# Optimization experiments

Hardware: AMD Instinct MI355X
Metric: run time of the kernel (lower is better)

The kernel has to match this reference:

```python
import jax, jax.numpy as jnp
import numpy as np

ALPHA, BETA, GAMMA, DELTA = 0.3, 0.3, 0.2, 0.2
BK, BW = 3, 3.0
EPS = 1e-7


def _bce_with_logits(x, y):
    # numerically stable: max(x,0) - x*y + log(1+exp(-|x|)); pos_weight=1.0
    return jnp.maximum(x, 0.0) - x * y + jnp.log1p(jnp.exp(-jnp.abs(x)))


def _lovasz_hinge_flat(x, y):
    # x, y: (N,) flattened logits / binary labels for one image
    signs = 2.0 * y - 1.0
    errors = 1.0 - x * signs
    perm = jnp.argsort(-errors)            # descending sort permutation
    errors_sorted = errors[perm]
    gt_sorted = y[perm]
    gts = gt_sorted.sum()
    intersection = gts - jnp.cumsum(gt_sorted)
    union = gts + jnp.cumsum(1.0 - gt_sorted)
    jaccard = 1.0 - intersection / union
    jaccard = jnp.concatenate([jaccard[:1], jaccard[1:] - jaccard[:-1]])
    return jnp.dot(jax.nn.relu(errors_sorted), jaccard)


def setup_inputs() -> dict:
    key = jax.random.key(0)
    k1, k2 = jax.random.split(key)
    logits = jax.random.normal(k1, (32, 1, 512, 512), dtype=jnp.float32)
    # binary ground-truth mask (0/1 floats)
    targets = jnp.round(jax.random.uniform(k2, (32, 1, 512, 512), dtype=jnp.float32))
    return {"logits": logits, "targets": targets}


def reference(logits, targets):
    # --- BCE term (pos_weight = 1.0) ---
    bce_elem = _bce_with_logits(logits, targets)
    bce = bce_elem.mean()

    # --- Dice term ---
    probs = jax.nn.sigmoid(logits)
    num = 2.0 * (probs * targets).sum(axis=(2, 3))
    den = (probs + targets).sum(axis=(2, 3)) + EPS
    dice = 1.0 - (num / den).mean()

    # --- Boundary-weighted BCE term (weights computed under no_grad) ---
    kernel = jnp.ones((1, 1, BK, BK), logits.dtype) / (BK * BK)
    smooth = jax.lax.conv_general_dilated(
        targets, kernel, window_strides=(1, 1), padding='SAME',
        dimension_numbers=('NCHW', 'OIHW', 'NCHW'))
    edges = ((smooth > 0.01) & (smooth < 0.99)).astype(logits.dtype)
    weights = jax.lax.stop_gradient(1.0 + edges * (BW - 1.0))
    boundary = (bce_elem * weights).mean()

    # --- Lovasz hinge, per image then averaged ---
    B = logits.shape[0]
    lov = jax.vmap(_lovasz_hinge_flat)(
        logits.reshape(B, -1), targets.reshape(B, -1)).mean()

    return ALPHA * bce + BETA * dice + GAMMA * boundary + DELTA * lov
```

## Files before the change

### kernel.cpp

```cpp
#include <hip/hip_runtime.h>
#include <hip/hip_bf16.h>


#define NB      32
#define HH      512
#define WW      512
#define HW      (HH*WW)
#define NTOT    (NB*HW)
#define K_BINS  1024
#define INV_H   128.0f
#define BIN_W   (1.0f/128.0f)

struct Ws {
    unsigned cnt[NB*K_BINS];
    float    sy[NB];
    float    spy[NB];
    float    Pim[NB];
    float    bce_sum;
    float    bceE_sum;
    float    lov_sum;
};

__device__ __forceinline__ void process_elem(float x, float y, float wsum,
                                             float& bce_s, float& bceE_s, float& sy_s,
                                             float& spy_s, float& P_s,
                                             unsigned* s_cnt) {
    const float ax = fabsf(x);
    const float t  = __expf(-ax);
    const float bce = fmaxf(x, 0.f) - x * y + __logf(1.f + t);
    const float inv = __builtin_amdgcn_rcpf(1.f + t);
    const float s = (x >= 0.f) ? inv : t * inv;
    const bool edge = (wsum > 0.5f) && (wsum < 8.5f);

    bce_s  += bce;
    bceE_s += edge ? bce : 0.f;
    sy_s   += s * y;
    spy_s  += s + y;
    P_s    += y;

    const float e = 1.f - x * (2.f * y - 1.f);
    if (e > 0.f) {
        int b = (int)(e * INV_H);
        if (b > K_BINS - 1) b = K_BINS - 1;
        atomicAdd(&s_cnt[b], (y > 0.5f) ? 0x10001u : 1u);
    }
}

__global__ __launch_bounds__(256, 2) void kernelA(const float* __restrict__ logits,
                                                  const float* __restrict__ targets,
                                                  Ws* __restrict__ ws) {
    __shared__ unsigned s_cnt[K_BINS];
    __shared__ float    red[4][5];

    const int tid  = threadIdx.x;
    const int lane = tid & 63;
    const int wave = tid >> 6;
    for (int i = tid; i < K_BINS; i += 256) s_cnt[i] = 0u;
    __syncthreads();

    const int img   = blockIdx.x >> 4;
    const int strip = ((blockIdx.x & 15) << 2) | wave;
    const int r0    = strip * 8;

    const float4* __restrict__ tg4 = (const float4*)(targets + img * HW);
    const float4* __restrict__ lg4 = (const float4*)(logits  + img * HW);
    const int cA = lane;
    const int cB = 64 + lane;

    float4 T[5][2]; float fT[5];
    float4 X[3][2];

#pragma unroll
    for (int s = 0; s < 5; ++s) {
        const int rr = r0 - 1 + s;
        const int rc = rr < 0 ? 0 : (rr > 511 ? 511 : rr);
        fT[s] = (rr >= 0 && rr < 512) ? 1.f : 0.f;
        T[s][0] = tg4[rc * 128 + cA];
        T[s][1] = tg4[rc * 128 + cB];
    }
#pragma unroll
    for (int s = 0; s < 3; ++s) {
        const int rr = r0 + s;
        X[s][0] = lg4[rr * 128 + cA];
        X[s][1] = lg4[rr * 128 + cB];
    }

    float bce_s = 0.f, bceE_s = 0.f, sy_s = 0.f, spy_s = 0.f, P_s = 0.f;

#pragma unroll
    for (int j = 0; j < 8; ++j) {
        const int ia = j % 5, ib = (j + 1) % 5, ic = (j + 2) % 5;
        const int xs = j % 3;
        const float fa = fT[ia], fc = fT[ic];

        float4 csA, csB;
        csA.x = fmaf(T[ia][0].x, fa, fmaf(T[ic][0].x, fc, T[ib][0].x));
        csA.y = fmaf(T[ia][0].y, fa, fmaf(T[ic][0].y, fc, T[ib][0].y));
        csA.z = fmaf(T[ia][0].z, fa, fmaf(T[ic][0].z, fc, T[ib][0].z));
        csA.w = fmaf(T[ia][0].w, fa, fmaf(T[ic][0].w, fc, T[ib][0].w));
        csB.x = fmaf(T[ia][1].x, fa, fmaf(T[ic][1].x, fc, T[ib][1].x));
        csB.y = fmaf(T[ia][1].y, fa, fmaf(T[ic][1].y, fc, T[ib][1].y));
        csB.z = fmaf(T[ia][1].z, fa, fmaf(T[ic][1].z, fc, T[ib][1].z));
        csB.w = fmaf(T[ia][1].w, fa, fmaf(T[ic][1].w, fc, T[ib][1].w));

        const float upA  = __shfl_up(csA.w, 1);
        const float dnA  = __shfl_down(csA.x, 1);
        const float upB  = __shfl_up(csB.w, 1);
        const float dnB  = __shfl_down(csB.x, 1);
        const float bc0  = __shfl(csB.x, 0);
        const float bc63 = __shfl(csA.w, 63);
        const float LA = (lane == 0)  ? 0.f  : upA;
        const float RA = (lane == 63) ? bc0  : dnA;
        const float LB = (lane == 0)  ? bc63 : upB;
        const float RB = (lane == 63) ? 0.f  : dnB;

        process_elem(X[xs][0].x, T[ib][0].x, LA + csA.x + csA.y,    bce_s, bceE_s, sy_s, spy_s, P_s, s_cnt);
        process_elem(X[xs][0].y, T[ib][0].y, csA.x + csA.y + csA.z, bce_s, bceE_s, sy_s, spy_s, P_s, s_cnt);
        process_elem(X[xs][0].z, T[ib][0].z, csA.y + csA.z + csA.w, bce_s, bceE_s, sy_s, spy_s, P_s, s_cnt);
        process_elem(X[xs][0].w, T[ib][0].w, csA.z + csA.w + RA,    bce_s, bceE_s, sy_s, spy_s, P_s, s_cnt);
        process_elem(X[xs][1].x, T[ib][1].x, LB + csB.x + csB.y,    bce_s, bceE_s, sy_s, spy_s, P_s, s_cnt);
        process_elem(X[xs][1].y, T[ib][1].y, csB.x + csB.y + csB.z, bce_s, bceE_s, sy_s, spy_s, P_s, s_cnt);
        process_elem(X[xs][1].z, T[ib][1].z, csB.y + csB.z + csB.w, bce_s, bceE_s, sy_s, spy_s, P_s, s_cnt);
        process_elem(X[xs][1].w, T[ib][1].w, csB.z + csB.w + RB,    bce_s, bceE_s, sy_s, spy_s, P_s, s_cnt);

        if (j < 5) {
            const int rr = r0 + j + 4;
            const int rc = rr > 511 ? 511 : rr;
            fT[ia] = (rr < 512) ? 1.f : 0.f;
            T[ia][0] = tg4[rc * 128 + cA];
            T[ia][1] = tg4[rc * 128 + cB];
            const int rx = r0 + j + 3;
            X[xs][0] = lg4[rx * 128 + cA];
            X[xs][1] = lg4[rx * 128 + cB];
        }
    }
    __syncthreads();

    unsigned* g_c = ws->cnt + img * K_BINS;
    for (int i = tid; i < K_BINS; i += 256) {
        const unsigned cpk = s_cnt[i];
        if (cpk) atomicAdd(&g_c[i], cpk);
    }

    for (int off = 32; off; off >>= 1) {
        bce_s  += __shfl_down(bce_s, off);
        bceE_s += __shfl_down(bceE_s, off);
        sy_s   += __shfl_down(sy_s, off);
        spy_s  += __shfl_down(spy_s, off);
        P_s    += __shfl_down(P_s, off);
    }
    if (lane == 0) {
        red[wave][0] = bce_s; red[wave][1] = bceE_s; red[wave][2] = sy_s;
        red[wave][3] = spy_s; red[wave][4] = P_s;
    }
    __syncthreads();
    if (tid == 0) {
        float a = 0.f, b = 0.f, c2 = 0.f, d = 0.f, e2 = 0.f;
        for (int w = 0; w < 4; ++w) {
            a += red[w][0]; b += red[w][1]; c2 += red[w][2];
            d += red[w][3]; e2 += red[w][4];
        }
        atomicAdd(&ws->bce_sum, a);
        atomicAdd(&ws->bceE_sum, b);
        atomicAdd(&ws->sy[img], c2);
        atomicAdd(&ws->spy[img], d);
        atomicAdd(&ws->Pim[img], e2);
    }
}

__global__ __launch_bounds__(256) void kernelB(Ws* __restrict__ ws) {
    __shared__ unsigned sc_a[256];
    __shared__ unsigned sc_p[256];
    __shared__ double   dred[4];

    const int img = blockIdx.x;
    const int tid = threadIdx.x;
    const unsigned* __restrict__ cn = ws->cnt + img * K_BINS;

    unsigned la[4], lp[4];
    float    me[4];
    unsigned tot_a = 0, tot_p = 0;
#pragma unroll
    for (int j = 0; j < 4; ++j) {
        const int k = K_BINS - 1 - (tid * 4 + j);
        const unsigned cpk = cn[k];
        la[j] = cpk & 0xFFFFu; lp[j] = cpk >> 16;
        me[j] = ((float)k + 0.5f) * BIN_W;
        tot_a += la[j]; tot_p += lp[j];
    }

    sc_a[tid] = tot_a; sc_p[tid] = tot_p;
    __syncthreads();
    for (int off = 1; off < 256; off <<= 1) {
        unsigned va = (tid >= off) ? sc_a[tid - off] : 0u;
        unsigned vp = (tid >= off) ? sc_p[tid - off] : 0u;
        __syncthreads();
        sc_a[tid] += va; sc_p[tid] += vp;
        __syncthreads();
    }
    const unsigned excl_a = sc_a[tid] - tot_a;
    const unsigned excl_p = sc_p[tid] - tot_p;

    const double P = (double)ws->Pim[img];
    double run_a = (double)excl_a, run_p = (double)excl_p;
    double contrib = 0.0;
#pragma unroll
    for (int j = 0; j < 4; ++j) {
        const double m = (double)la[j];
        const double p = (double)lp[j];
        if (la[j]) {
            const double u = P + (run_a + 0.5 * m) - (run_p + 0.5 * p);
            const double c = run_p + 0.5 * p;
            contrib += (double)(lp[j] * me[j]) / u;
            const double den = u * (u - 1.0);
            if (den > 0.0)
                contrib += (double)((la[j] - lp[j]) * me[j]) * (P - c) / den;
        }
        run_a += m; run_p += p;
    }

    for (int off = 32; off; off >>= 1) contrib += __shfl_down(contrib, off);
    const int wave = tid >> 6;
    const int lane = tid & 63;
    if (lane == 0) dred[wave] = contrib;
    __syncthreads();
    if (tid == 0) {
        double tot = dred[0] + dred[1] + dred[2] + dred[3];
        atomicAdd(&ws->lov_sum, (float)tot);
    }
}

__global__ __launch_bounds__(64) void kernelC(const Ws* __restrict__ ws,
                                              float* __restrict__ out) {
    const int lane = threadIdx.x;
    float dsum = 0.f;
    if (lane < NB) {
        const float num = 2.f * ws->sy[lane];
        const float den = ws->spy[lane] + 1e-7f;
        dsum = num / den;
    }
    for (int off = 32; off; off >>= 1) dsum += __shfl_down(dsum, off);
    if (lane == 0) {
        const float invN = 1.f / (float)NTOT;
        const float bce      = ws->bce_sum * invN;
        const float boundary = (ws->bce_sum + 2.f * ws->bceE_sum) * invN;
        const float dice     = 1.f - dsum / (float)NB;
        const float lov      = ws->lov_sum / (float)NB;
        out[0] = 0.3f * bce + 0.3f * dice + 0.2f * boundary + 0.2f * lov;
    }
}

extern "C" void kernel_launch(void* const* d_in, const int* in_sizes, int n_in,
                              void* d_out, int out_size, void* d_ws, size_t ws_size,
                              hipStream_t stream) {
    const float* logits  = (const float*)d_in[0];
    const float* targets = (const float*)d_in[1];
    float* out = (float*)d_out;
    Ws* ws = (Ws*)d_ws;

    (void)hipMemsetAsync(d_ws, 0, sizeof(Ws), stream);
    kernelA<<<NB * 16, 256, 0, stream>>>(logits, targets, ws);
    kernelB<<<NB, 256, 0, stream>>>(ws);
    kernelC<<<1, 64, 0, stream>>>(ws, out);
}
```

Measured before the change: 116.0 us.

## Replace global atomics and memset with per-block partials and fused finalize

Kernel A now writes each block's histogram and five scalar partials to private workspace slots instead of doing global atomics, so the memset is no longer needed. The histogram and lovasz kernel reduces the 16 per-block histograms and partials itself, and a ticket counter lets the last block compute the final loss, which removes the third kernel launch. This cuts atomic contention, one memset and one launch. In exchange the workspace is larger, the second kernel does 16 times more histogram reads, and resetting the ticket from block 0 of kernel A depends on launch ordering.

```diff
diff --git a/kernel.cpp b/kernel.cpp
--- a/kernel.cpp
+++ b/kernel.cpp
@@ -10,15 +10,13 @@
 #define K_BINS  1024
 #define INV_H   128.0f
 #define BIN_W   (1.0f/128.0f)
+#define BPI     16
 
 struct Ws {
-    unsigned cnt[NB*K_BINS];
-    float    sy[NB];
-    float    spy[NB];
-    float    Pim[NB];
-    float    bce_sum;
-    float    bceE_sum;
-    float    lov_sum;
+    unsigned cnt[NB*BPI*K_BINS];
+    float    partf[NB*BPI*5];
+    float4   vals[NB];
+    unsigned ticket;
 };
 
 __device__ __forceinline__ void process_elem(float x, float y, float wsum,
@@ -136,11 +134,8 @@
     }
     __syncthreads();
 
-    unsigned* g_c = ws->cnt + img * K_BINS;
-    for (int i = tid; i < K_BINS; i += 256) {
-        const unsigned cpk = s_cnt[i];
-        if (cpk) atomicAdd(&g_c[i], cpk);
-    }
+    unsigned* g_c = ws->cnt + blockIdx.x * K_BINS;
+    for (int i = tid; i < K_BINS; i += 256) g_c[i] = s_cnt[i];
 
     for (int off = 32; off; off >>= 1) {
         bce_s  += __shfl_down(bce_s, off);
@@ -160,33 +155,62 @@
             a += red[w][0]; b += red[w][1]; c2 += red[w][2];
             d += red[w][3]; e2 += red[w][4];
         }
-        atomicAdd(&ws->bce_sum, a);
-        atomicAdd(&ws->bceE_sum, b);
-        atomicAdd(&ws->sy[img], c2);
-        atomicAdd(&ws->spy[img], d);
-        atomicAdd(&ws->Pim[img], e2);
-    }
-}
-
-__global__ __launch_bounds__(256) void kernelB(Ws* __restrict__ ws) {
+        float* pf = ws->partf + blockIdx.x * 5;
+        pf[0] = a; pf[1] = b; pf[2] = c2; pf[3] = d; pf[4] = e2;
+        if (blockIdx.x == 0) ws->ticket = 0u;
+    }
+}
+
+__global__ __launch_bounds__(256) void kernelBC(Ws* __restrict__ ws,
+                                                float* __restrict__ out) {
     __shared__ unsigned sc_a[256];
     __shared__ unsigned sc_p[256];
     __shared__ double   dred[4];
+    __shared__ float    s_P, s_bce, s_bceE, s_dice;
+    __shared__ int      s_last;
 
     const int img = blockIdx.x;
     const int tid = threadIdx.x;
-    const unsigned* __restrict__ cn = ws->cnt + img * K_BINS;
-
+
+    float pf0 = 0.f, pf1 = 0.f, pf2 = 0.f, pf3 = 0.f, pf4 = 0.f;
+    if (tid < BPI) {
+        const float* p = ws->partf + (img * BPI + tid) * 5;
+        pf0 = p[0]; pf1 = p[1]; pf2 = p[2]; pf3 = p[3]; pf4 = p[4];
+    }
+    if (tid < 64) {
+        for (int off = 8; off; off >>= 1) {
+            pf0 += __shfl_down(pf0, off);
+            pf1 += __shfl_down(pf1, off);
+            pf2 += __shfl_down(pf2, off);
+            pf3 += __shfl_down(pf3, off);
+            pf4 += __shfl_down(pf4, off);
+        }
+        if (tid == 0) {
+            s_bce  = pf0;
+            s_bceE = pf1;
+            s_dice = 2.f * pf2 / (pf3 + 1e-7f);
+            s_P    = pf4;
+        }
+    }
+    __syncthreads();
+
+    const unsigned* __restrict__ cn = ws->cnt + img * BPI * K_BINS;
     unsigned la[4], lp[4];
     float    me[4];
     unsigned tot_a = 0, tot_p = 0;
 #pragma unroll
     for (int j = 0; j < 4; ++j) {
         const int k = K_BINS - 1 - (tid * 4 + j);
-        const unsigned cpk = cn[k];
-        la[j] = cpk & 0xFFFFu; lp[j] = cpk >> 16;
+        unsigned a = 0, p = 0;
+#pragma unroll
+        for (int b = 0; b < BPI; ++b) {
+            const unsigned cpk = cn[b * K_BINS + k];
+            a += cpk & 0xFFFFu;
+            p += cpk >> 16;
+        }
+        la[j] = a; lp[j] = p;
         me[j] = ((float)k + 0.5f) * BIN_W;
-        tot_a += la[j]; tot_p += lp[j];
+        tot_a += a; tot_p += p;
     }
 
     sc_a[tid] = tot_a; sc_p[tid] = tot_p;
@@ -201,7 +225,7 @@
     const unsigned excl_a = sc_a[tid] - tot_a;
     const unsigned excl_p = sc_p[tid] - tot_p;
 
-    const double P = (double)ws->Pim[img];
+    const double P = (double)s_P;
     double run_a = (double)excl_a, run_p = (double)excl_p;
     double contrib = 0.0;
 #pragma unroll
@@ -224,29 +248,41 @@
     const int lane = tid & 63;
     if (lane == 0) dred[wave] = contrib;
     __syncthreads();
+
     if (tid == 0) {
-        double tot = dred[0] + dred[1] + dred[2] + dred[3];
-        atomicAdd(&ws->lov_sum, (float)tot);
-    }
-}
-
-__global__ __launch_bounds__(64) void kernelC(const Ws* __restrict__ ws,
-                                              float* __restrict__ out) {
-    const int lane = threadIdx.x;
-    float dsum = 0.f;
-    if (lane < NB) {
-        const float num = 2.f * ws->sy[lane];
-        const float den = ws->spy[lane] + 1e-7f;
-        dsum = num / den;
-    }
-    for (int off = 32; off; off >>= 1) dsum += __shfl_down(dsum, off);
-    if (lane == 0) {
-        const float invN = 1.f / (float)NTOT;
-        const float bce      = ws->bce_sum * invN;
-        const float boundary = (ws->bce_sum + 2.f * ws->bceE_sum) * invN;
-        const float dice     = 1.f - dsum / (float)NB;
-        const float lov      = ws->lov_sum / (float)NB;
-        out[0] = 0.3f * bce + 0.3f * dice + 0.2f * boundary + 0.2f * lov;
+        const double tot = dred[0] + dred[1] + dred[2] + dred[3];
+        float4 v;
+        v.x = s_bce; v.y = s_bceE; v.z = s_dice; v.w = (float)tot;
+        ws->vals[img] = v;
+        __threadfence();
+        const unsigned old = atomicAdd(&ws->ticket, 1u);
+        s_last = (old == NB - 1) ? 1 : 0;
+    }
+    __syncthreads();
+
+    if (s_last) {
+        __threadfence();
+        if (tid < 64) {
+            float vx = 0.f, vy = 0.f, vz = 0.f, vw = 0.f;
+            if (tid < NB) {
+                const float4 v = ws->vals[tid];
+                vx = v.x; vy = v.y; vz = v.z; vw = v.w;
+            }
+            for (int off = 16; off; off >>= 1) {
+                vx += __shfl_down(vx, off);
+                vy += __shfl_down(vy, off);
+                vz += __shfl_down(vz, off);
+                vw += __shfl_down(vw, off);
+            }
+            if (tid == 0) {
+                const float invN = 1.f / (float)NTOT;
+                const float bce      = vx * invN;
+                const float boundary = (vx + 2.f * vy) * invN;
+                const float dice     = 1.f - vz / (float)NB;
+                const float lov      = vw / (float)NB;
+                out[0] = 0.3f * bce + 0.3f * dice + 0.2f * boundary + 0.2f * lov;
+            }
+        }
     }
 }
 
@@ -258,8 +294,6 @@
     float* out = (float*)d_out;
     Ws* ws = (Ws*)d_ws;
 
-    (void)hipMemsetAsync(d_ws, 0, sizeof(Ws), stream);
-    kernelA<<<NB * 16, 256, 0, stream>>>(logits, targets, ws);
-    kernelB<<<NB, 256, 0, stream>>>(ws);
-    kernelC<<<1, 64, 0, stream>>>(ws, out);
-}
+    kernelA<<<NB * BPI, 256, 0, stream>>>(logits, targets, ws);
+    kernelBC<<<NB, 256, 0, stream>>>(ws, out);
+}
```

Measured after the change: 108.0 us. 6.9% less time.
